# Kernel optimization log

Hardware: AMD Instinct MI355X
Metric: run time of the kernel (lower is better)

## Reference

```python
import jax, jax.numpy as jnp
import numpy as np

WS = 7       # window_size
SHIFT = 3    # shift_size
NH = 4       # num_heads


def _layernorm(x, g, b, eps=1e-5):
    m = jnp.mean(x, axis=-1, keepdims=True)
    v = jnp.mean((x - m) ** 2, axis=-1, keepdims=True)
    return (x - m) * jax.lax.rsqrt(v + eps) * g + b


def _mha(x, wq, bq, wk, bk, wv, bv, wo, bo):
    # x: [n, s, c]; weights stored as [in, out]
    n, s, c = x.shape
    dk = c // NH
    q = (x @ wq + bq).reshape(n, s, NH, dk).transpose(0, 2, 1, 3)
    k = (x @ wk + bk).reshape(n, s, NH, dk).transpose(0, 2, 1, 3)
    v = (x @ wv + bv).reshape(n, s, NH, dk).transpose(0, 2, 1, 3)
    scores = jnp.einsum('nhqd,nhkd->nhqk', q, k) / jnp.sqrt(jnp.float32(dk))
    attn = jax.nn.softmax(scores, axis=-1)  # dropout is identity in eval
    out = jnp.einsum('nhqk,nhkd->nhqd', attn, v)
    out = out.transpose(0, 2, 1, 3).reshape(n, s, c)
    return out @ wo + bo


def _window_partition(x):
    B, H, W, C = x.shape
    x = x.reshape(B, H // WS, WS, W // WS, WS, C)
    x = x.transpose(0, 1, 3, 2, 4, 5)
    return x.reshape(-1, WS * WS, C)


def _window_reverse(wins, H, W):
    C = wins.shape[-1]
    B = wins.shape[0] // ((H // WS) * (W // WS))
    x = wins.reshape(B, H // WS, W // WS, WS, WS, C)
    x = x.transpose(0, 1, 3, 2, 4, 5)
    return x.reshape(B, H, W, C)


def setup_inputs() -> dict:
    key = jax.random.key(0)
    ks = jax.random.split(key, 16)
    C = 128
    def w(k, shape):
        return jax.random.normal(k, shape, dtype=jnp.float32) * 0.02
    return {
        'x':  jax.random.normal(ks[0], (4, 56, 56, C), dtype=jnp.float32),
        'wq': w(ks[1], (C, C)), 'bq': jnp.zeros((C,), jnp.float32),
        'wk': w(ks[2], (C, C)), 'bk': jnp.zeros((C,), jnp.float32),
        'wv': w(ks[3], (C, C)), 'bv': jnp.zeros((C,), jnp.float32),
        'wo': w(ks[4], (C, C)), 'bo': jnp.zeros((C,), jnp.float32),
        'w1': w(ks[5], (C, 4 * C)), 'b1': jnp.zeros((4 * C,), jnp.float32),
        'w2': w(ks[6], (4 * C, C)), 'b2': jnp.zeros((C,), jnp.float32),
        'g1': jnp.ones((C,), jnp.float32), 'be1': jnp.zeros((C,), jnp.float32),
        'g2': jnp.ones((C,), jnp.float32), 'be2': jnp.zeros((C,), jnp.float32),
    }


def reference(x, wq, bq, wk, bk, wv, bv, wo, bo, w1, b1, w2, b2, g1, be1, g2, be2):
    B, H, W, C = x.shape
    # cyclic shift
    xs = jnp.roll(x, shift=(-SHIFT, -SHIFT), axis=(1, 2)) if SHIFT > 0 else x
    # windowed attention (note: original code replaces x, no residual here)
    wins = _window_partition(xs)                         # [B*nW, 49, C]
    attn_wins = _mha(wins, wq, bq, wk, bk, wv, bv, wo, bo)
    xs = _window_reverse(attn_wins, H, W)
    x = jnp.roll(xs, shift=(SHIFT, SHIFT), axis=(1, 2)) if SHIFT > 0 else xs
    # global attention residual branch (flatten H*W tokens)
    xf = x.reshape(B, H * W, C)
    xf = xf + _mha(_layernorm(xf, g1, be1), wq, bq, wk, bk, wv, bv, wo, bo)
    # MLP residual branch
    h = jax.nn.gelu(_layernorm(xf, g2, be2) @ w1 + b1, approximate=False)
    xf = xf + (h @ w2 + b2)
    return xf.reshape(B, H, W, C)
```

## Files before the change

### kernel.cpp

```cpp
#include <hip/hip_runtime.h>
#include <hip/hip_bf16.h>
#include <math.h>

#define NH 4
#define DK 32
#define CC 128
#define HW 56
#define SHIFT 3
#define NTOK 12544
#define S_GLB 3136
#define VTW_STRIDE 12608
#define SCALE_L2E 0.25503488f

typedef unsigned short u16;
typedef short bf16x8 __attribute__((ext_vector_type(8)));
typedef unsigned short u16x8 __attribute__((ext_vector_type(8)));
typedef float f32x4 __attribute__((ext_vector_type(4)));

static __device__ __forceinline__ u16 f2bf(float f) {
  unsigned int b = __builtin_bit_cast(unsigned int, f);
  return (u16)((b + 0x7FFFu + ((b >> 16) & 1u)) >> 16);
}
static __device__ __forceinline__ unsigned pk2bf(float a, float b) {
  unsigned r;
  asm("v_cvt_pk_bf16_f32 %0, %1, %2" : "=v"(r) : "v"(a), "v"(b));
  return r;
}
static __device__ __forceinline__ float fexp2(float x) {
  float r;
  asm("v_exp_f32 %0, %1" : "=v"(r) : "v"(x));
  return r;
}
static __device__ __forceinline__ void gload16(const void* g, void* l) {
  __builtin_amdgcn_global_load_lds(
      (const __attribute__((address_space(1))) unsigned int*)g,
      (__attribute__((address_space(3))) unsigned int*)l, 16, 0, 0);
}

__global__ __launch_bounds__(256) void cvt_all_k(
    const float* __restrict__ w1, const float* __restrict__ w2,
    const float* __restrict__ wq, const float* __restrict__ wk,
    const float* __restrict__ wv, const float* __restrict__ wo,
    u16* __restrict__ w1t, u16* __restrict__ w2t,
    u16* __restrict__ wqkvt, u16* __restrict__ wot) {
  const int idx = blockIdx.x * 256 + threadIdx.x;
  if (idx < 65536) {
    const int c = idx >> 7, r = idx & 127;
    w1t[idx] = f2bf(w1[r * 512 + c]);
  } else if (idx < 131072) {
    const int o = idx - 65536;
    const int c = o / 512, r = o - c * 512;
    w2t[o] = f2bf(w2[r * 128 + c]);
  } else {
    const int o = idx - 131072;
    const int which = o >> 14, oo = o & 16383;
    const int c = oo >> 7, r = oo & 127;
    const float* src = (which == 0) ? wq : (which == 1) ? wk : (which == 2) ? wv : wo;
    u16* dst = (which < 3) ? (wqkvt + which * 16384) : wot;
    dst[oo] = f2bf(src[r * 128 + c]);
  }
}

__global__ __launch_bounds__(256) void win_gather_k(
    const float* __restrict__ x, u16* __restrict__ xg) {
  const int t = blockIdx.x * 2 + (threadIdx.x >> 7);
  const int c = threadIdx.x & 127;
  const int win = t / 49, tok = t % 49;
  const int b = win >> 6, wrem = win & 63;
  const int wi = wrem >> 3, wj = wrem & 7;
  const int i = tok / 7, j = tok % 7;
  int hh = wi * 7 + i + SHIFT; if (hh >= HW) hh -= HW;
  int ww = wj * 7 + j + SHIFT; if (ww >= HW) ww -= HW;
  xg[(size_t)t * CC + c] = f2bf(x[((size_t)(b * HW + hh) * HW + ww) * CC + c]);
}

__global__ __launch_bounds__(128) void ln_k(
    const float* __restrict__ xf, const float* __restrict__ g,
    const float* __restrict__ be, u16* __restrict__ ybf) {
  __shared__ float xs[8][CC];
  __shared__ float red[8][2];
  const int t0 = blockIdx.x * 8;
  const int tid = threadIdx.x;
  for (int t2 = 0; t2 < 8; ++t2) xs[t2][tid] = xf[(size_t)(t0 + t2) * CC + tid];
  __syncthreads();
  const int wvi = tid >> 6, lane = tid & 63;
  for (int t2 = wvi * 4; t2 < wvi * 4 + 4; ++t2) {
    const float v0 = xs[t2][lane], v1 = xs[t2][64 + lane];
    float s = v0 + v1, sq = v0 * v0 + v1 * v1;
#pragma unroll
    for (int off = 1; off < 64; off <<= 1) { s += __shfl_xor(s, off); sq += __shfl_xor(sq, off); }
    if (lane == 0) {
      const float mu = s * 0.0078125f;
      const float var = sq * 0.0078125f - mu * mu;
      red[t2][0] = mu; red[t2][1] = rsqrtf(var + 1e-5f);
    }
  }
  __syncthreads();
  const float gg = g[tid], bb = be[tid];
  for (int t2 = 0; t2 < 8; ++t2)
    ybf[(size_t)(t0 + t2) * CC + tid] = f2bf((xs[t2][tid] - red[t2][0]) * red[t2][1] * gg + bb);
}

template <int PATH>
__global__ __launch_bounds__(256) void qkv_gemm_k(
    const u16* __restrict__ xin, const u16* __restrict__ wqkvt,
    const float* __restrict__ bq, const float* __restrict__ bk,
    const float* __restrict__ bv,
    u16* __restrict__ qo, u16* __restrict__ ko, u16* __restrict__ vto) {
  __shared__ __align__(16) u16 xs[64][136];
  __shared__ __align__(16) u16 wt[64][136];
  const int tid = threadIdx.x;
  const int w = tid >> 6, lane = tid & 63;
  const int lo = lane & 15, hi = lane >> 4, hi4 = hi * 4;
  const int m0 = blockIdx.x * 64;
  const int widx = blockIdx.y >> 1;
  const int n0 = (blockIdx.y & 1) * 64;
  {
    const int r = tid >> 2, sg = tid & 3;
    const u16* sx = &xin[(size_t)(m0 + r) * CC + sg * 32];
    const u16* sw = &wqkvt[(size_t)widx * CC * CC + (size_t)(n0 + r) * CC + sg * 32];
#pragma unroll
    for (int j = 0; j < 4; ++j) {
      *reinterpret_cast<u16x8*>(&xs[r][sg * 32 + j * 8]) = *reinterpret_cast<const u16x8*>(&sx[j * 8]);
      *reinterpret_cast<u16x8*>(&wt[r][sg * 32 + j * 8]) = *reinterpret_cast<const u16x8*>(&sw[j * 8]);
    }
  }
  __syncthreads();
  if (widx < 2) {
    const float* bias = (widx == 0) ? bq : bk;
    u16* outp = (widx == 0) ? qo : ko;
    const float oscale = (widx == 0) ? SCALE_L2E : 1.0f;
    f32x4 acc[4];
#pragma unroll
    for (int st = 0; st < 4; ++st) {
      const float b_ = bias[n0 + st * 16 + lo];
      acc[st] = (f32x4){b_, b_, b_, b_};
    }
#pragma unroll
    for (int kk = 0; kk < 4; ++kk) {
      const bf16x8 af = *reinterpret_cast<const bf16x8*>(&xs[w * 16 + lo][kk * 32 + 8 * hi]);
#pragma unroll
      for (int st = 0; st < 4; ++st) {
        const bf16x8 bfr = *reinterpret_cast<const bf16x8*>(&wt[st * 16 + lo][kk * 32 + 8 * hi]);
        acc[st] = __builtin_amdgcn_mfma_f32_16x16x32_bf16(af, bfr, acc[st], 0, 0, 0);
      }
    }
#pragma unroll
    for (int r = 0; r < 4; ++r) {
      const int mm = m0 + w * 16 + hi4 + r;
      size_t rowbase, hstride;
      if (PATH == 0) {
        const int win = mm / 49, tok = mm - win * 49;
        rowbase = ((size_t)(win * 4) * 49 + tok) * DK;
        hstride = (size_t)49 * DK;
      } else {
        const int b = mm / S_GLB, s = mm - b * S_GLB;
        rowbase = ((size_t)(b * 4) * S_GLB + s) * DK;
        hstride = (size_t)S_GLB * DK;
      }
#pragma unroll
      for (int st = 0; st < 4; ++st) {
        const int c = n0 + st * 16 + lo, h = c >> 5, d = c & 31;
        outp[rowbase + (size_t)h * hstride + d] = f2bf(acc[st][r] * oscale);
      }
    }
  } else {
    f32x4 bias4;
#pragma unroll
    for (int r = 0; r < 4; ++r) bias4[r] = bv[n0 + w * 16 + hi4 + r];
    f32x4 acc[4];
#pragma unroll
    for (int st = 0; st < 4; ++st) acc[st] = bias4;
#pragma unroll
    for (int kk = 0; kk < 4; ++kk) {
      const bf16x8 af = *reinterpret_cast<const bf16x8*>(&wt[w * 16 + lo][kk * 32 + 8 * hi]);
#pragma unroll
      for (int st = 0; st < 4; ++st) {
        const bf16x8 bfr = *reinterpret_cast<const bf16x8*>(&xs[st * 16 + lo][kk * 32 + 8 * hi]);
        acc[st] = __builtin_amdgcn_mfma_f32_16x16x32_bf16(af, bfr, acc[st], 0, 0, 0);
      }
    }
#pragma unroll
    for (int st = 0; st < 4; ++st) {
      const int mm = m0 + st * 16 + lo;
#pragma unroll
      for (int r = 0; r < 4; ++r) {
        const int c = n0 + w * 16 + hi4 + r;
        if (PATH == 0) {
          vto[(size_t)c * VTW_STRIDE + mm] = f2bf(acc[st][r]);
        } else {
          const int b = mm / S_GLB, s = mm - b * S_GLB;
          vto[((size_t)b * CC + c) * S_GLB + s] = f2bf(acc[st][r]);
        }
      }
    }
  }
}

__global__ __launch_bounds__(256) void win_attn_k(
    const u16* __restrict__ qw, const u16* __restrict__ kw,
    const u16* __restrict__ vtw, u16* __restrict__ aow) {
  __shared__ __align__(16) u16 psh[4][16][72];
  const int tid = threadIdx.x;
  const int wvi = tid >> 6, lane = tid & 63;
  const int lo = lane & 15, hi = lane >> 4, hi4 = hi * 4;
  const int wh = blockIdx.x * 4 + wvi;
  const int win = wh >> 2, hd = wh & 3;
  const f32x4 zero4 = {0.f, 0.f, 0.f, 0.f};
  bf16x8 ones;
#pragma unroll
  for (int j = 0; j < 8; ++j) ones[j] = (short)0x3F80;

  bf16x8 kf[4], vf[2][2];
#pragma unroll
  for (int st = 0; st < 4; ++st)
    kf[st] = *reinterpret_cast<const bf16x8*>(&kw[((size_t)wh * 49 + st * 16 + lo) * DK + 8 * hi]);
#pragma unroll
  for (int dst = 0; dst < 2; ++dst)
#pragma unroll
    for (int kch = 0; kch < 2; ++kch)
      vf[dst][kch] = *reinterpret_cast<const bf16x8*>(
          &vtw[(size_t)(hd * DK + dst * 16 + lo) * VTW_STRIDE + win * 49 + kch * 32 + 8 * hi]);

#pragma unroll
  for (int g = 0; g < 4; ++g) {
    const bf16x8 qf = *reinterpret_cast<const bf16x8*>(
        &qw[((size_t)wh * 49 + g * 16 + lo) * DK + 8 * hi]);
    f32x4 s4[4];
#pragma unroll
    for (int st = 0; st < 4; ++st) {
      s4[st] = __builtin_amdgcn_mfma_f32_16x16x32_bf16(kf[st], qf, zero4, 0, 0, 0);
#pragma unroll
      for (int r = 0; r < 4; ++r)
        if (st * 16 + hi4 + r >= 49) s4[st][r] = -1e30f;
    }
#pragma unroll
    for (int st = 0; st < 4; ++st) {
      uint2 pk;
      pk.x = pk2bf(fexp2(s4[st][0]), fexp2(s4[st][1]));
      pk.y = pk2bf(fexp2(s4[st][2]), fexp2(s4[st][3]));
      *reinterpret_cast<uint2*>(&psh[wvi][lo][st * 16 + hi4]) = pk;
    }
    asm volatile("" ::: "memory");
    f32x4 acc0 = zero4, acc1 = zero4, lacc = zero4;
#pragma unroll
    for (int kch = 0; kch < 2; ++kch) {
      const bf16x8 pa = *reinterpret_cast<const bf16x8*>(&psh[wvi][lo][kch * 32 + 8 * hi]);
      acc0 = __builtin_amdgcn_mfma_f32_16x16x32_bf16(pa, vf[0][kch], acc0, 0, 0, 0);
      acc1 = __builtin_amdgcn_mfma_f32_16x16x32_bf16(pa, vf[1][kch], acc1, 0, 0, 0);
      lacc = __builtin_amdgcn_mfma_f32_16x16x32_bf16(pa, ones, lacc, 0, 0, 0);
    }
#pragma unroll
    for (int r = 0; r < 4; ++r) {
      const int qrow = g * 16 + hi4 + r;
      if (qrow < 49) {
        const float rl = 1.0f / lacc[r];
        const size_t tw = (size_t)win * 49 + qrow;
        aow[tw * CC + hd * DK + lo] = f2bf(acc0[r] * rl);
        aow[tw * CC + hd * DK + 16 + lo] = f2bf(acc1[r] * rl);
      }
    }
  }
}

__global__ __launch_bounds__(256) void glb_attn_k(
    const u16* __restrict__ qg, const u16* __restrict__ kg,
    const u16* __restrict__ vtg, float* __restrict__ po, float* __restrict__ pl) {
  __shared__ __align__(16) u16 ksh[2][64][32];
  __shared__ __align__(16) u16 vtsh[2][32][64];
  __shared__ __align__(16) u16 psh[4][16][64];
  const int tid = threadIdx.x;
  const int w = tid >> 6, lane = tid & 63;
  const int lo = lane & 15, hi = lane >> 4, hi4 = hi * 4;
  const int bh = blockIdx.y;
  const int q0 = blockIdx.x * 64;
  const int sp = blockIdx.z;
  const int kt_beg = sp * 25;
  const int kt_end = sp ? 49 : 25;
  const f32x4 zero4 = {0.f, 0.f, 0.f, 0.f};
  bf16x8 ones;
#pragma unroll
  for (int j = 0; j < 8; ++j) ones[j] = (short)0x3F80;

  const bf16x8 qfrag = *reinterpret_cast<const bf16x8*>(
      &qg[((size_t)bh * S_GLB + q0 + w * 16 + lo) * DK + 8 * hi]);
  const u16* kg0 = kg + (size_t)bh * S_GLB * DK;
  const u16* vg0 = vtg + (size_t)bh * DK * S_GLB;

  const u16* ksrc = kg0 + (size_t)(w * 16 + (lane >> 2)) * DK + (lane & 3) * 8;
  const u16* vsrc = vg0 + (size_t)(w * 8 + (lane >> 3)) * S_GLB + ((lane & 7) ^ (lane >> 3)) * 8;
  u16* kdst0 = &ksh[0][w * 16][0]; u16* kdst1 = &ksh[1][w * 16][0];
  u16* vdst0 = &vtsh[0][w * 8][0]; u16* vdst1 = &vtsh[1][w * 8][0];

  f32x4 oacc0 = zero4, oacc1 = zero4, lacc = zero4;

  gload16(ksrc + (size_t)kt_beg * 64 * DK, kdst0);
  gload16(vsrc + (size_t)kt_beg * 64, vdst0);
  __syncthreads();

  char* const pbase = (char*)&psh[w][lo][0];
  char* const vbase0 = (char*)&vtsh[0][0][0];
  const unsigned swz = (unsigned)(lo & 7) << 4;

  for (int kt = kt_beg; kt < kt_end; ++kt) {
    const int cur = (kt - kt_beg) & 1;
    if (kt + 1 < kt_end) {
      gload16(ksrc + (size_t)(kt + 1) * 64 * DK, cur ? kdst0 : kdst1);
      gload16(vsrc + (size_t)(kt + 1) * 64, cur ? vdst0 : vdst1);
    }
    f32x4 s4[4];
#pragma unroll
    for (int st = 0; st < 4; ++st) {
      const bf16x8 kfrag = *reinterpret_cast<const bf16x8*>(&ksh[cur][st * 16 + lo][8 * hi]);
      s4[st] = __builtin_amdgcn_mfma_f32_16x16x32_bf16(kfrag, qfrag, zero4, 0, 0, 0);
    }
#pragma unroll
    for (int st = 0; st < 4; ++st) {
      uint2 pk;
      pk.x = pk2bf(fexp2(s4[st][0]), fexp2(s4[st][1]));
      pk.y = pk2bf(fexp2(s4[st][2]), fexp2(s4[st][3]));
      *reinterpret_cast<uint2*>(pbase + (((unsigned)(st * 32 + hi * 8)) ^ swz)) = pk;
    }
    asm volatile("" ::: "memory");
    char* const vrow0 = vbase0 + (size_t)cur * (32 * 64 * 2) + lo * 128;
#pragma unroll
    for (int kch = 0; kch < 2; ++kch) {
      const unsigned off = ((unsigned)(kch * 64 + hi * 16)) ^ swz;
      const bf16x8 pa = *reinterpret_cast<const bf16x8*>(pbase + off);
      const bf16x8 v0 = *reinterpret_cast<const bf16x8*>(vrow0 + off);
      const bf16x8 v1 = *reinterpret_cast<const bf16x8*>(vrow0 + 16 * 128 + off);
      oacc0 = __builtin_amdgcn_mfma_f32_16x16x32_bf16(pa, v0, oacc0, 0, 0, 0);
      oacc1 = __builtin_amdgcn_mfma_f32_16x16x32_bf16(pa, v1, oacc1, 0, 0, 0);
      lacc = __builtin_amdgcn_mfma_f32_16x16x32_bf16(pa, ones, lacc, 0, 0, 0);
    }
    __syncthreads();
  }

  const int b = bh >> 2, hd = bh & 3;
  float* pob = po + (size_t)sp * NTOK * CC;
#pragma unroll
  for (int r = 0; r < 4; ++r) {
    const size_t t = (size_t)b * S_GLB + q0 + w * 16 + hi4 + r;
    pob[t * CC + hd * DK + lo] = oacc0[r];
    pob[t * CC + hd * DK + 16 + lo] = oacc1[r];
    if (lo == 0)
      pl[((size_t)sp * 16 + bh) * S_GLB + q0 + w * 16 + hi4 + r] = lacc[r];
  }
}

__global__ __launch_bounds__(256) void combine_k(
    const float* __restrict__ po, const float* __restrict__ pl,
    u16* __restrict__ aog) {
  const int t = blockIdx.x * 2 + (threadIdx.x >> 7);
  const int c = threadIdx.x & 127;
  const int b = t / S_GLB, s = t - b * S_GLB;
  const int bh = b * 4 + (c >> 5);
  const float l = pl[(size_t)bh * S_GLB + s] + pl[((size_t)16 + bh) * S_GLB + s];
  const float v = po[(size_t)t * CC + c] + po[(size_t)NTOK * CC + (size_t)t * CC + c];
  aog[(size_t)t * CC + c] = f2bf(v / l);
}

template <int MODE>
__global__ __launch_bounds__(256) void proj_gemm_k(
    const u16* __restrict__ ain, const u16* __restrict__ wot,
    const float* __restrict__ bo, const float* __restrict__ resid,
    float* __restrict__ xfo) {
  __shared__ __align__(16) u16 xs[64][136];
  __shared__ __align__(16) u16 wt[64][136];
  const int tid = threadIdx.x;
  const int w = tid >> 6, lane = tid & 63;
  const int lo = lane & 15, hi = lane >> 4, hi4 = hi * 4;
  const int m0 = blockIdx.x * 64;
  const int n0 = blockIdx.y * 64;
  {
    const int r = tid >> 2, sg = tid & 3;
    const u16* sx = &ain[(size_t)(m0 + r) * CC + sg * 32];
    const u16* sw = &wot[(size_t)(n0 + r) * CC + sg * 32];
#pragma unroll
    for (int j = 0; j < 4; ++j) {
      *reinterpret_cast<u16x8*>(&xs[r][sg * 32 + j * 8]) = *reinterpret_cast<const u16x8*>(&sx[j * 8]);
      *reinterpret_cast<u16x8*>(&wt[r][sg * 32 + j * 8]) = *reinterpret_cast<const u16x8*>(&sw[j * 8]);
    }
  }
  __syncthreads();
  f32x4 acc[4];
#pragma unroll
  for (int st = 0; st < 4; ++st) {
    const float b_ = bo[n0 + st * 16 + lo];
    acc[st] = (f32x4){b_, b_, b_, b_};
  }
#pragma unroll
  for (int kk = 0; kk < 4; ++kk) {
    const bf16x8 af = *reinterpret_cast<const bf16x8*>(&xs[w * 16 + lo][kk * 32 + 8 * hi]);
#pragma unroll
    for (int st = 0; st < 4; ++st) {
      const bf16x8 bfr = *reinterpret_cast<const bf16x8*>(&wt[st * 16 + lo][kk * 32 + 8 * hi]);
      acc[st] = __builtin_amdgcn_mfma_f32_16x16x32_bf16(af, bfr, acc[st], 0, 0, 0);
    }
  }
#pragma unroll
  for (int r = 0; r < 4; ++r) {
    const int mm = m0 + w * 16 + hi4 + r;
    size_t trow;
    if (MODE == 0) {
      const int win = mm / 49, tok = mm - win * 49;
      const int b = win >> 6, wi = (win >> 3) & 7, wj = win & 7;
      const int ii = tok / 7, jj = tok - ii * 7;
      int hr = wi * 7 + ii + SHIFT; if (hr >= HW) hr -= HW;
      int wr = wj * 7 + jj + SHIFT; if (wr >= HW) wr -= HW;
      trow = ((size_t)b * S_GLB + hr * HW + wr) * CC;
    } else {
      trow = (size_t)mm * CC;
    }
#pragma unroll
    for (int st = 0; st < 4; ++st) {
      const int c = n0 + st * 16 + lo;
      if (MODE == 1)
        xfo[trow + c] = resid[trow + c] + acc[st][r];
      else
        xfo[trow + c] = acc[st][r];
    }
  }
}

__global__ __launch_bounds__(256) void gemm1_k(
    const u16* __restrict__ ybf, const u16* __restrict__ w1t,
    const float* __restrict__ b1, u16* __restrict__ hb) {
  __shared__ __align__(16) u16 xs[64][136];
  __shared__ __align__(16) u16 wt[64][136];
  const int tid = threadIdx.x;
  const int w = tid >> 6, lane = tid & 63;
  const int lo = lane & 15, hi = lane >> 4;
  const int m0 = blockIdx.x * 64, n0 = blockIdx.y * 64;
  {
    const int r = tid >> 2, sg = tid & 3;
    const u16* src_x = &ybf[(size_t)(m0 + r) * CC + sg * 32];
    const u16* src_w = &w1t[(size_t)(n0 + r) * CC + sg * 32];
#pragma unroll
    for (int j = 0; j < 4; ++j) {
      *reinterpret_cast<u16x8*>(&xs[r][sg * 32 + j * 8]) = *reinterpret_cast<const u16x8*>(&src_x[j * 8]);
      *reinterpret_cast<u16x8*>(&wt[r][sg * 32 + j * 8]) = *reinterpret_cast<const u16x8*>(&src_w[j * 8]);
    }
  }
  __syncthreads();
  f32x4 acc[4];
#pragma unroll
  for (int st = 0; st < 4; ++st) {
    const float bv = b1[n0 + st * 16 + lo];
    acc[st] = (f32x4){bv, bv, bv, bv};
  }
#pragma unroll
  for (int kk = 0; kk < 4; ++kk) {
    const bf16x8 af = *reinterpret_cast<const bf16x8*>(&xs[w * 16 + lo][kk * 32 + 8 * hi]);
#pragma unroll
    for (int st = 0; st < 4; ++st) {
      const bf16x8 bfr = *reinterpret_cast<const bf16x8*>(&wt[st * 16 + lo][kk * 32 + 8 * hi]);
      acc[st] = __builtin_amdgcn_mfma_f32_16x16x32_bf16(af, bfr, acc[st], 0, 0, 0);
    }
  }
#pragma unroll
  for (int st = 0; st < 4; ++st) {
#pragma unroll
    for (int r = 0; r < 4; ++r) {
      const float val = acc[st][r];
      const float gel = 0.5f * val * (1.0f + erff(val * 0.70710678118f));
      hb[(size_t)(m0 + w * 16 + (hi << 2) + r) * 512 + n0 + st * 16 + lo] = f2bf(gel);
    }
  }
}

__global__ __launch_bounds__(256) void gemm2_k(
    const u16* __restrict__ hb, const u16* __restrict__ w2t,
    const float* __restrict__ b2, const float* __restrict__ xf,
    float* __restrict__ out) {
  __shared__ __align__(16) u16 xs[64][136];
  __shared__ __align__(16) u16 wt[64][136];
  const int tid = threadIdx.x;
  const int w = tid >> 6, lane = tid & 63;
  const int lo = lane & 15, hi = lane >> 4;
  const int m0 = blockIdx.x * 64, n0 = blockIdx.y * 64;
  f32x4 acc[4];
#pragma unroll
  for (int st = 0; st < 4; ++st) {
    const float bv = b2[n0 + st * 16 + lo];
    acc[st] = (f32x4){bv, bv, bv, bv};
  }
  for (int kc = 0; kc < 4; ++kc) {
    if (kc) __syncthreads();
    {
      const int r = tid >> 2, sg = tid & 3;
      const u16* src_x = &hb[(size_t)(m0 + r) * 512 + kc * 128 + sg * 32];
      const u16* src_w = &w2t[(size_t)(n0 + r) * 512 + kc * 128 + sg * 32];
#pragma unroll
      for (int j = 0; j < 4; ++j) {
        *reinterpret_cast<u16x8*>(&xs[r][sg * 32 + j * 8]) = *reinterpret_cast<const u16x8*>(&src_x[j * 8]);
        *reinterpret_cast<u16x8*>(&wt[r][sg * 32 + j * 8]) = *reinterpret_cast<const u16x8*>(&src_w[j * 8]);
      }
    }
    __syncthreads();
#pragma unroll
    for (int kk = 0; kk < 4; ++kk) {
      const bf16x8 af = *reinterpret_cast<const bf16x8*>(&xs[w * 16 + lo][kk * 32 + 8 * hi]);
#pragma unroll
      for (int st = 0; st < 4; ++st) {
        const bf16x8 bfr = *reinterpret_cast<const bf16x8*>(&wt[st * 16 + lo][kk * 32 + 8 * hi]);
        acc[st] = __builtin_amdgcn_mfma_f32_16x16x32_bf16(af, bfr, acc[st], 0, 0, 0);
      }
    }
  }
#pragma unroll
  for (int st = 0; st < 4; ++st) {
#pragma unroll
    for (int r = 0; r < 4; ++r) {
      const size_t idx = (size_t)(m0 + w * 16 + (hi << 2) + r) * CC + n0 + st * 16 + lo;
      out[idx] = xf[idx] + acc[st][r];
    }
  }
}

extern "C" void kernel_launch(void* const* d_in, const int* in_sizes, int n_in,
                              void* d_out, int out_size, void* d_ws, size_t ws_size,
                              hipStream_t stream) {
  (void)in_sizes; (void)n_in; (void)out_size; (void)ws_size;
  const float* x   = (const float*)d_in[0];
  const float* wq  = (const float*)d_in[1];
  const float* bq  = (const float*)d_in[2];
  const float* wk  = (const float*)d_in[3];
  const float* bk  = (const float*)d_in[4];
  const float* wv  = (const float*)d_in[5];
  const float* bv  = (const float*)d_in[6];
  const float* wo  = (const float*)d_in[7];
  const float* bo  = (const float*)d_in[8];
  const float* w1  = (const float*)d_in[9];
  const float* b1  = (const float*)d_in[10];
  const float* w2  = (const float*)d_in[11];
  const float* b2  = (const float*)d_in[12];
  const float* g1  = (const float*)d_in[13];
  const float* be1 = (const float*)d_in[14];
  const float* g2  = (const float*)d_in[15];
  const float* be2 = (const float*)d_in[16];
  float* out = (float*)d_out;

  char* p = (char*)d_ws;
  auto alloc = [&](size_t bytes) { char* r = p; p += (bytes + 255) & ~(size_t)255; return r; };
  float* xf  = (float*)alloc((size_t)NTOK * CC * 4);
  u16* xg    = (u16*)alloc((size_t)NTOK * CC * 2);
  u16* qw    = (u16*)alloc((size_t)NTOK * CC * 2 + 4096);
  u16* kw    = (u16*)alloc((size_t)NTOK * CC * 2 + 4096);
  u16* vtw   = (u16*)alloc((size_t)CC * VTW_STRIDE * 2);
  u16* aow   = (u16*)alloc((size_t)NTOK * CC * 2);
  u16* hb    = (u16*)alloc((size_t)NTOK * 512 * 2);
  float* po  = (float*)alloc((size_t)2 * NTOK * CC * 4);
  float* pl  = (float*)alloc((size_t)2 * 16 * S_GLB * 4);
  u16* wqkvt = (u16*)alloc(3 * 16384 * 2);
  u16* wot   = (u16*)alloc(16384 * 2);
  u16* w1t   = (u16*)alloc(65536 * 2);
  u16* w2t   = (u16*)alloc(65536 * 2);

  cvt_all_k<<<768, 256, 0, stream>>>(w1, w2, wq, wk, wv, wo, w1t, w2t, wqkvt, wot);

  win_gather_k<<<NTOK / 2, 256, 0, stream>>>(x, xg);
  qkv_gemm_k<0><<<dim3(NTOK / 64, 6), 256, 0, stream>>>(xg, wqkvt, bq, bk, bv, qw, kw, vtw);
  win_attn_k<<<256, 256, 0, stream>>>(qw, kw, vtw, aow);
  proj_gemm_k<0><<<dim3(NTOK / 64, 2), 256, 0, stream>>>(aow, wot, bo, nullptr, xf);

  ln_k<<<NTOK / 8, 128, 0, stream>>>(xf, g1, be1, xg);
  qkv_gemm_k<1><<<dim3(NTOK / 64, 6), 256, 0, stream>>>(xg, wqkvt, bq, bk, bv, qw, kw, vtw);
  glb_attn_k<<<dim3(S_GLB / 64, 16, 2), 256, 0, stream>>>(qw, kw, vtw, po, pl);
  combine_k<<<NTOK / 2, 256, 0, stream>>>(po, pl, aow);
  proj_gemm_k<1><<<dim3(NTOK / 64, 2), 256, 0, stream>>>(aow, wot, bo, xf, xf);

  ln_k<<<NTOK / 8, 128, 0, stream>>>(xf, g2, be2, xg);
  gemm1_k<<<dim3(NTOK / 64, 8), 256, 0, stream>>>(xg, w1t, b1, hb);
  gemm2_k<<<dim3(NTOK / 64, 2), 256, 0, stream>>>(hb, w2t, b2, xf, out);
}
```

Baseline: 123.3 us.

## Fuse split-K combine and LayerNorm into output projection, merge prep kernels

Merges weight conversion and the window gather into one launch. Folds the split-K attention combine into the second output projection and fuses LayerNorm into both projection epilogues, so each block now computes all 128 output channels. This removes three kernel launches and the fp32 round trips through xf for the separate LN passes. In exchange there is half as many projection blocks, more LDS (128-row weight tile) and more registers per block, plus in-place read/write of xf in MODE 1.

```diff
diff --git a/kernel.cpp b/kernel.cpp
--- a/kernel.cpp
+++ b/kernel.cpp
@@ -37,68 +37,42 @@
       (__attribute__((address_space(3))) unsigned int*)l, 16, 0, 0);
 }
 
-__global__ __launch_bounds__(256) void cvt_all_k(
+__global__ __launch_bounds__(256) void prep_k(
     const float* __restrict__ w1, const float* __restrict__ w2,
     const float* __restrict__ wq, const float* __restrict__ wk,
     const float* __restrict__ wv, const float* __restrict__ wo,
+    const float* __restrict__ x,
     u16* __restrict__ w1t, u16* __restrict__ w2t,
-    u16* __restrict__ wqkvt, u16* __restrict__ wot) {
-  const int idx = blockIdx.x * 256 + threadIdx.x;
-  if (idx < 65536) {
-    const int c = idx >> 7, r = idx & 127;
-    w1t[idx] = f2bf(w1[r * 512 + c]);
-  } else if (idx < 131072) {
-    const int o = idx - 65536;
-    const int c = o / 512, r = o - c * 512;
-    w2t[o] = f2bf(w2[r * 128 + c]);
+    u16* __restrict__ wqkvt, u16* __restrict__ wot, u16* __restrict__ xg) {
+  if (blockIdx.x < 768) {
+    const int idx = blockIdx.x * 256 + threadIdx.x;
+    if (idx < 65536) {
+      const int c = idx >> 7, r = idx & 127;
+      w1t[idx] = f2bf(w1[r * 512 + c]);
+    } else if (idx < 131072) {
+      const int o = idx - 65536;
+      const int c = o / 512, r = o - c * 512;
+      w2t[o] = f2bf(w2[r * 128 + c]);
+    } else {
+      const int o = idx - 131072;
+      const int which = o >> 14, oo = o & 16383;
+      const int c = oo >> 7, r = oo & 127;
+      const float* src = (which == 0) ? wq : (which == 1) ? wk : (which == 2) ? wv : wo;
+      u16* dst = (which < 3) ? (wqkvt + which * 16384) : wot;
+      dst[oo] = f2bf(src[r * 128 + c]);
+    }
   } else {
-    const int o = idx - 131072;
-    const int which = o >> 14, oo = o & 16383;
-    const int c = oo >> 7, r = oo & 127;
-    const float* src = (which == 0) ? wq : (which == 1) ? wk : (which == 2) ? wv : wo;
-    u16* dst = (which < 3) ? (wqkvt + which * 16384) : wot;
-    dst[oo] = f2bf(src[r * 128 + c]);
-  }
-}
-
-__global__ __launch_bounds__(256) void win_gather_k(
-    const float* __restrict__ x, u16* __restrict__ xg) {
-  const int t = blockIdx.x * 2 + (threadIdx.x >> 7);
-  const int c = threadIdx.x & 127;
-  const int win = t / 49, tok = t % 49;
-  const int b = win >> 6, wrem = win & 63;
-  const int wi = wrem >> 3, wj = wrem & 7;
-  const int i = tok / 7, j = tok % 7;
-  int hh = wi * 7 + i + SHIFT; if (hh >= HW) hh -= HW;
-  int ww = wj * 7 + j + SHIFT; if (ww >= HW) ww -= HW;
-  xg[(size_t)t * CC + c] = f2bf(x[((size_t)(b * HW + hh) * HW + ww) * CC + c]);
-}
-
-__global__ __launch_bounds__(128) void ln_k(
-    const float* __restrict__ xf, const float* __restrict__ g,
-    const float* __restrict__ be, u16* __restrict__ ybf) {
-  __shared__ float xs[8][CC];
-  __shared__ float red[8][2];
-  const int t0 = blockIdx.x * 8;
-  const int tid = threadIdx.x;
-  for (int t2 = 0; t2 < 8; ++t2) xs[t2][tid] = xf[(size_t)(t0 + t2) * CC + tid];
-  __syncthreads();
-  const int wvi = tid >> 6, lane = tid & 63;
-  for (int t2 = wvi * 4; t2 < wvi * 4 + 4; ++t2) {
-    const float v0 = xs[t2][lane], v1 = xs[t2][64 + lane];
-    float s = v0 + v1, sq = v0 * v0 + v1 * v1;
-#pragma unroll
-    for (int off = 1; off < 64; off <<= 1) { s += __shfl_xor(s, off); sq += __shfl_xor(sq, off); }
-    if (lane == 0) {
-      const float mu = s * 0.0078125f;
-      const float var = sq * 0.0078125f - mu * mu;
-      red[t2][0] = mu; red[t2][1] = rsqrtf(var + 1e-5f);
-    }
-  }
-  __syncthreads();
-  const float gg = g[tid], bb = be[tid];
-  for (int t2 = 0; t2 < 8; ++t2)
-    ybf[(size_t)(t0 + t2) * CC + tid] = f2bf((xs[t2][tid] - red[t2][0]) * red[t2][1] * gg + bb);
+    const int bid = blockIdx.x - 768;
+    const int t = bid * 2 + (threadIdx.x >> 7);
+    const int c = threadIdx.x & 127;
+    const int win = t / 49, tok = t % 49;
+    const int b = win >> 6, wrem = win & 63;
+    const int wi = wrem >> 3, wj = wrem & 7;
+    const int i = tok / 7, j = tok % 7;
+    int hh = wi * 7 + i + SHIFT; if (hh >= HW) hh -= HW;
+    int ww = wj * 7 + j + SHIFT; if (ww >= HW) ww -= HW;
+    xg[(size_t)t * CC + c] = f2bf(x[((size_t)(b * HW + hh) * HW + ww) * CC + c]);
+  }
 }
 
 template <int PATH>
@@ -348,56 +322,69 @@
   }
 }
 
-__global__ __launch_bounds__(256) void combine_k(
-    const float* __restrict__ po, const float* __restrict__ pl,
-    u16* __restrict__ aog) {
-  const int t = blockIdx.x * 2 + (threadIdx.x >> 7);
-  const int c = threadIdx.x & 127;
-  const int b = t / S_GLB, s = t - b * S_GLB;
-  const int bh = b * 4 + (c >> 5);
-  const float l = pl[(size_t)bh * S_GLB + s] + pl[((size_t)16 + bh) * S_GLB + s];
-  const float v = po[(size_t)t * CC + c] + po[(size_t)NTOK * CC + (size_t)t * CC + c];
-  aog[(size_t)t * CC + c] = f2bf(v / l);
-}
-
 template <int MODE>
-__global__ __launch_bounds__(256) void proj_gemm_k(
-    const u16* __restrict__ ain, const u16* __restrict__ wot,
+__global__ __launch_bounds__(256) void proj_ln_k(
+    const u16* __restrict__ ain, const float* __restrict__ po,
+    const float* __restrict__ pl, const u16* __restrict__ wot,
     const float* __restrict__ bo, const float* __restrict__ resid,
-    float* __restrict__ xfo) {
+    const float* __restrict__ lng, const float* __restrict__ lnb,
+    float* __restrict__ xfo, u16* __restrict__ ybf) {
   __shared__ __align__(16) u16 xs[64][136];
-  __shared__ __align__(16) u16 wt[64][136];
+  __shared__ __align__(16) u16 wt[128][136];
   const int tid = threadIdx.x;
   const int w = tid >> 6, lane = tid & 63;
   const int lo = lane & 15, hi = lane >> 4, hi4 = hi * 4;
   const int m0 = blockIdx.x * 64;
-  const int n0 = blockIdx.y * 64;
   {
     const int r = tid >> 2, sg = tid & 3;
-    const u16* sx = &ain[(size_t)(m0 + r) * CC + sg * 32];
-    const u16* sw = &wot[(size_t)(n0 + r) * CC + sg * 32];
-#pragma unroll
-    for (int j = 0; j < 4; ++j) {
-      *reinterpret_cast<u16x8*>(&xs[r][sg * 32 + j * 8]) = *reinterpret_cast<const u16x8*>(&sx[j * 8]);
-      *reinterpret_cast<u16x8*>(&wt[r][sg * 32 + j * 8]) = *reinterpret_cast<const u16x8*>(&sw[j * 8]);
-    }
+    if (MODE == 0) {
+      const u16* sx = &ain[(size_t)(m0 + r) * CC + sg * 32];
+#pragma unroll
+      for (int j = 0; j < 4; ++j)
+        *reinterpret_cast<u16x8*>(&xs[r][sg * 32 + j * 8]) = *reinterpret_cast<const u16x8*>(&sx[j * 8]);
+    } else {
+      const int mm = m0 + r;
+      const int b = mm / S_GLB, s_ = mm - b * S_GLB;
+      const float l0 = pl[((size_t)(b * 4 + sg)) * S_GLB + s_];
+      const float l1 = pl[((size_t)(16 + b * 4 + sg)) * S_GLB + s_];
+      const float rl = 1.0f / (l0 + l1);
+      const float* pa = &po[(size_t)mm * CC + sg * 32];
+      const float* pb = pa + (size_t)NTOK * CC;
+#pragma unroll
+      for (int j = 0; j < 32; j += 4) {
+        const float4 a4 = *reinterpret_cast<const float4*>(&pa[j]);
+        const float4 b4 = *reinterpret_cast<const float4*>(&pb[j]);
+        uint2 pk;
+        pk.x = pk2bf((a4.x + b4.x) * rl, (a4.y + b4.y) * rl);
+        pk.y = pk2bf((a4.z + b4.z) * rl, (a4.w + b4.w) * rl);
+        *reinterpret_cast<uint2*>(&xs[r][sg * 32 + j]) = pk;
+      }
+    }
+    const int r2 = tid >> 1, sg2 = tid & 1;
+    const u16* sw = &wot[(size_t)r2 * CC + sg2 * 64];
+#pragma unroll
+    for (int j = 0; j < 8; ++j)
+      *reinterpret_cast<u16x8*>(&wt[r2][sg2 * 64 + j * 8]) = *reinterpret_cast<const u16x8*>(&sw[j * 8]);
   }
   __syncthreads();
-  f32x4 acc[4];
-#pragma unroll
-  for (int st = 0; st < 4; ++st) {
-    const float b_ = bo[n0 + st * 16 + lo];
+  f32x4 acc[8];
+#pragma unroll
+  for (int st = 0; st < 8; ++st) {
+    const float b_ = bo[st * 16 + lo];
     acc[st] = (f32x4){b_, b_, b_, b_};
   }
 #pragma unroll
   for (int kk = 0; kk < 4; ++kk) {
     const bf16x8 af = *reinterpret_cast<const bf16x8*>(&xs[w * 16 + lo][kk * 32 + 8 * hi]);
 #pragma unroll
-    for (int st = 0; st < 4; ++st) {
+    for (int st = 0; st < 8; ++st) {
       const bf16x8 bfr = *reinterpret_cast<const bf16x8*>(&wt[st * 16 + lo][kk * 32 + 8 * hi]);
       acc[st] = __builtin_amdgcn_mfma_f32_16x16x32_bf16(af, bfr, acc[st], 0, 0, 0);
     }
   }
+  float gv[8], bv2[8];
+#pragma unroll
+  for (int st = 0; st < 8; ++st) { gv[st] = lng[st * 16 + lo]; bv2[st] = lnb[st * 16 + lo]; }
 #pragma unroll
   for (int r = 0; r < 4; ++r) {
     const int mm = m0 + w * 16 + hi4 + r;
@@ -408,17 +395,29 @@
       const int ii = tok / 7, jj = tok - ii * 7;
       int hr = wi * 7 + ii + SHIFT; if (hr >= HW) hr -= HW;
       int wr = wj * 7 + jj + SHIFT; if (wr >= HW) wr -= HW;
-      trow = ((size_t)b * S_GLB + hr * HW + wr) * CC;
+      trow = (size_t)b * S_GLB + hr * HW + wr;
     } else {
-      trow = (size_t)mm * CC;
-    }
-#pragma unroll
-    for (int st = 0; st < 4; ++st) {
-      const int c = n0 + st * 16 + lo;
-      if (MODE == 1)
-        xfo[trow + c] = resid[trow + c] + acc[st][r];
-      else
-        xfo[trow + c] = acc[st][r];
+      trow = (size_t)mm;
+    }
+    float v[8];
+    float s = 0.f, sq = 0.f;
+#pragma unroll
+    for (int st = 0; st < 8; ++st) {
+      float t_ = acc[st][r];
+      if (MODE == 1) t_ += resid[trow * CC + st * 16 + lo];
+      v[st] = t_;
+      s += t_;
+      sq += t_ * t_;
+    }
+    s += __shfl_xor(s, 1); s += __shfl_xor(s, 2); s += __shfl_xor(s, 4); s += __shfl_xor(s, 8);
+    sq += __shfl_xor(sq, 1); sq += __shfl_xor(sq, 2); sq += __shfl_xor(sq, 4); sq += __shfl_xor(sq, 8);
+    const float mu = s * 0.0078125f;
+    const float rsig = rsqrtf(sq * 0.0078125f - mu * mu + 1e-5f);
+#pragma unroll
+    for (int st = 0; st < 8; ++st) {
+      const size_t idx = trow * CC + st * 16 + lo;
+      xfo[idx] = v[st];
+      ybf[idx] = f2bf((v[st] - mu) * rsig * gv[st] + bv2[st]);
     }
   }
 }
@@ -557,20 +556,16 @@
   u16* w1t   = (u16*)alloc(65536 * 2);
   u16* w2t   = (u16*)alloc(65536 * 2);
 
-  cvt_all_k<<<768, 256, 0, stream>>>(w1, w2, wq, wk, wv, wo, w1t, w2t, wqkvt, wot);
-
-  win_gather_k<<<NTOK / 2, 256, 0, stream>>>(x, xg);
+  prep_k<<<768 + NTOK / 2, 256, 0, stream>>>(
+      w1, w2, wq, wk, wv, wo, x, w1t, w2t, wqkvt, wot, xg);
   qkv_gemm_k<0><<<dim3(NTOK / 64, 6), 256, 0, stream>>>(xg, wqkvt, bq, bk, bv, qw, kw, vtw);
   win_attn_k<<<256, 256, 0, stream>>>(qw, kw, vtw, aow);
-  proj_gemm_k<0><<<dim3(NTOK / 64, 2), 256, 0, stream>>>(aow, wot, bo, nullptr, xf);
-
-  ln_k<<<NTOK / 8, 128, 0, stream>>>(xf, g1, be1, xg);
+  proj_ln_k<0><<<NTOK / 64, 256, 0, stream>>>(
+      aow, nullptr, nullptr, wot, bo, nullptr, g1, be1, xf, xg);
   qkv_gemm_k<1><<<dim3(NTOK / 64, 6), 256, 0, stream>>>(xg, wqkvt, bq, bk, bv, qw, kw, vtw);
   glb_attn_k<<<dim3(S_GLB / 64, 16, 2), 256, 0, stream>>>(qw, kw, vtw, po, pl);
-  combine_k<<<NTOK / 2, 256, 0, stream>>>(po, pl, aow);
-  proj_gemm_k<1><<<dim3(NTOK / 64, 2), 256, 0, stream>>>(aow, wot, bo, xf, xf);
-
-  ln_k<<<NTOK / 8, 128, 0, stream>>>(xf, g2, be2, xg);
+  proj_ln_k<1><<<NTOK / 64, 256, 0, stream>>>(
+      nullptr, po, pl, wot, bo, xf, g2, be2, xf, xg);
   gemm1_k<<<dim3(NTOK / 64, 8), 256, 0, stream>>>(xg, w1t, b1, hb);
   gemm2_k<<<dim3(NTOK / 64, 2), 256, 0, stream>>>(hb, w2t, b2, xf, out);
 }
```

New measurement: 111.4 us. -9.7%, faster.
